# Kernel optimization log

Hardware: AMD Instinct MI355X
Metric: run time of the kernel (lower is better)

The kernel has to match this reference:

```python
import jax, jax.numpy as jnp
import numpy as np

N_NODES = 10000
N_EDGES = 320000
F_IN = 128
HID = 32


def sage_mean(x, src, dst, W_self, W_neigh, b, n_nodes):
    # mean aggregation over in-neighbors (messages flow src -> dst)
    msg = x[src]                                   # [E, F]
    agg = jax.ops.segment_sum(msg, dst, num_segments=n_nodes)   # [N, F]
    deg = jax.ops.segment_sum(jnp.ones((src.shape[0],), x.dtype), dst,
                              num_segments=n_nodes)             # [N]
    h_neigh = agg / jnp.maximum(deg, 1.0)[:, None]
    return x @ W_self + h_neigh @ W_neigh + b


def setup_inputs() -> dict:
    key = jax.random.key(0)
    ks = jax.random.split(key, 12)
    s = 0.05
    return {
        "n_feats": jax.random.normal(ks[0], (N_NODES, F_IN), jnp.float32),
        "src": jax.random.randint(ks[1], (N_EDGES,), 0, N_NODES, jnp.int32),
        "dst": jax.random.randint(ks[2], (N_EDGES,), 0, N_NODES, jnp.int32),
        "eps": jax.random.normal(ks[3], (N_NODES, HID), jnp.float32),
        "W1_self": jax.random.normal(ks[4], (F_IN, HID), jnp.float32) * s,
        "W1_neigh": jax.random.normal(ks[5], (F_IN, HID), jnp.float32) * s,
        "b1": jnp.zeros((HID,), jnp.float32),
        "Wmu_self": jax.random.normal(ks[6], (HID, HID), jnp.float32) * s,
        "Wmu_neigh": jax.random.normal(ks[7], (HID, HID), jnp.float32) * s,
        "bmu": jnp.zeros((HID,), jnp.float32),
        "Wls_self": jax.random.normal(ks[8], (HID, HID), jnp.float32) * s,
        "Wls_neigh": jax.random.normal(ks[9], (HID, HID), jnp.float32) * s,
        "bls": jnp.zeros((HID,), jnp.float32),
    }


def reference(n_feats, src, dst, eps, W1_self, W1_neigh, b1,
              Wmu_self, Wmu_neigh, bmu, Wls_self, Wls_neigh, bls):
    n = n_feats.shape[0]
    h = jax.nn.relu(sage_mean(n_feats, src, dst, W1_self, W1_neigh, b1, n))
    mu = sage_mean(h, src, dst, Wmu_self, Wmu_neigh, bmu, n)
    logstd = sage_mean(h, src, dst, Wls_self, Wls_neigh, bls, n)
    z = mu + eps * jnp.exp(logstd)          # reparameterize
    adj = jax.nn.sigmoid(z @ z.T)           # dot-product decode, [N, N]
    return adj, mu, logstd
```

## Files before the change

kernel.cpp:

```cpp
#include <hip/hip_runtime.h>
#include <hip/hip_bf16.h>


#define N_NODES 10000
#define N_EDGES 320000
#define F_IN 128
#define HID 32

__global__ __launch_bounds__(256) void k_gemm_in(
    const float* __restrict__ x, const float* __restrict__ Ws,
    const float* __restrict__ Wn, const float* __restrict__ b,
    float* __restrict__ outS, float* __restrict__ outN) {
  __shared__ float sWs[F_IN * HID];
  __shared__ float sWn[F_IN * HID];
  __shared__ float sx[8 * F_IN];
  const int t = threadIdx.x;
  for (int i = t * 4; i < F_IN * HID; i += 1024) {
    *(float4*)&sWs[i] = *(const float4*)&Ws[i];
    *(float4*)&sWn[i] = *(const float4*)&Wn[i];
  }
  const int row0 = blockIdx.x * 8;
  {
    const int i = t * 4;
    const int r = i >> 7, k = i & 127;
    const int gr = row0 + r;
    float4 v = make_float4(0.f, 0.f, 0.f, 0.f);
    if (gr < N_NODES) v = *(const float4*)&x[gr * F_IN + k];
    *(float4*)&sx[i] = v;
  }
  __syncthreads();
  const int r = t >> 5, c = t & 31;
  const int grow = row0 + r;
  float accS = 0.f, accN = 0.f;
  #pragma unroll 8
  for (int k = 0; k < F_IN; ++k) {
    const float a = sx[r * F_IN + k];
    accS += a * sWs[k * HID + c];
    accN += a * sWn[k * HID + c];
  }
  if (grow < N_NODES) {
    outS[grow * HID + c] = accS + b[c];
    outN[grow * HID + c] = accN;
  }
}

__global__ __launch_bounds__(256) void k_aggregate(
    const float* __restrict__ feat, const int* __restrict__ src,
    const int* __restrict__ dst, float* __restrict__ agg,
    float* __restrict__ deg) {
  const int tid = blockIdx.x * 256 + threadIdx.x;
  const int e = tid >> 5;
  const int k = tid & 31;
  if (e >= N_EDGES) return;
  const int s = src[e];
  const int d = dst[e];
  atomicAdd(&agg[d * HID + k], feat[s * HID + k]);
  if (deg != nullptr && k == 0) atomicAdd(&deg[d], 1.0f);
}

__global__ __launch_bounds__(256) void k_layer1_finish(
    const float* __restrict__ xws, const float* __restrict__ agg,
    const float* __restrict__ deg, float* __restrict__ h) {
  const int i = blockIdx.x * 256 + threadIdx.x;
  if (i >= N_NODES * HID) return;
  const int node = i >> 5;
  float dv = deg[node];
  dv = dv > 1.f ? dv : 1.f;
  const float v = xws[i] + agg[i] / dv;
  h[i] = v > 0.f ? v : 0.f;
}

__global__ __launch_bounds__(256) void k_layer2(
    const float* __restrict__ h, const float* __restrict__ aggh,
    const float* __restrict__ deg, const float* __restrict__ eps,
    const float* __restrict__ Wms, const float* __restrict__ Wmn,
    const float* __restrict__ bm, const float* __restrict__ Wls,
    const float* __restrict__ Wln, const float* __restrict__ bl,
    float* __restrict__ mu_out, float* __restrict__ ls_out,
    float* __restrict__ z) {
  __shared__ float sMs[HID * HID], sMn[HID * HID];
  __shared__ float sLs[HID * HID], sLn[HID * HID];
  __shared__ float sh[8 * HID], shn[8 * HID];
  const int t = threadIdx.x;
  {
    const int i = t * 4;
    *(float4*)&sMs[i] = *(const float4*)&Wms[i];
    *(float4*)&sMn[i] = *(const float4*)&Wmn[i];
    *(float4*)&sLs[i] = *(const float4*)&Wls[i];
    *(float4*)&sLn[i] = *(const float4*)&Wln[i];
  }
  const int node0 = blockIdx.x * 8;
  const int lr = t >> 5;
  const int gnode_ld = node0 + lr;
  if (gnode_ld < N_NODES) {
    float dv = deg[gnode_ld];
    dv = dv > 1.f ? dv : 1.f;
    sh[t] = h[node0 * HID + t];
    shn[t] = aggh[node0 * HID + t] / dv;
  } else {
    sh[t] = 0.f;
    shn[t] = 0.f;
  }
  __syncthreads();
  const int r = t >> 5, c = t & 31;
  const int node = node0 + r;
  float mu = 0.f, ls = 0.f;
  #pragma unroll 8
  for (int k = 0; k < HID; ++k) {
    const float a = sh[r * HID + k];
    const float an = shn[r * HID + k];
    mu += a * sMs[k * HID + c] + an * sMn[k * HID + c];
    ls += a * sLs[k * HID + c] + an * sLn[k * HID + c];
  }
  if (node < N_NODES) {
    mu += bm[c];
    ls += bl[c];
    const int idx = node * HID + c;
    mu_out[idx] = mu;
    ls_out[idx] = ls;
    z[idx] = mu + eps[idx] * __expf(ls);
  }
}

__global__ __launch_bounds__(256) void k_decode(const float* __restrict__ z,
                                                float* __restrict__ adj) {
  __shared__ float za[128][36];
  __shared__ float zb[128][36];
  const int r0 = blockIdx.y * 128;
  const int c0 = blockIdx.x * 128;
  const int t = threadIdx.x;
  for (int i = t; i < 128 * 8; i += 256) {
    const int row = i >> 3, k0 = (i & 7) << 2;
    const int gr = r0 + row;
    const int gc = c0 + row;
    float4 va = make_float4(0.f, 0.f, 0.f, 0.f);
    float4 vb = make_float4(0.f, 0.f, 0.f, 0.f);
    if (gr < N_NODES) va = *(const float4*)&z[gr * HID + k0];
    if (gc < N_NODES) vb = *(const float4*)&z[gc * HID + k0];
    *(float4*)&za[row][k0] = va;
    *(float4*)&zb[row][k0] = vb;
  }
  __syncthreads();
  const int tx = t & 15, ty = t >> 4;
  float acc[8][8];
  #pragma unroll
  for (int i = 0; i < 8; ++i)
    #pragma unroll
    for (int j = 0; j < 8; ++j) acc[i][j] = 0.f;

  #pragma unroll 4
  for (int k = 0; k < HID; ++k) {
    float a[8], b[8];
    #pragma unroll
    for (int i = 0; i < 8; ++i) a[i] = za[ty + i * 16][k];
    #pragma unroll
    for (int j = 0; j < 8; ++j) b[j] = zb[tx + j * 16][k];
    #pragma unroll
    for (int i = 0; i < 8; ++i)
      #pragma unroll
      for (int j = 0; j < 8; ++j) acc[i][j] += a[i] * b[j];
  }

  #pragma unroll
  for (int i = 0; i < 8; ++i) {
    const int r = r0 + ty + i * 16;
    if (r >= N_NODES) continue;
    float* rowp = adj + (size_t)r * N_NODES;
    #pragma unroll
    for (int j = 0; j < 8; ++j) {
      const int c = c0 + tx + j * 16;
      if (c < N_NODES) {
        const float v = acc[i][j];
        rowp[c] = __builtin_amdgcn_rcpf(1.f + __expf(-v));
      }
    }
  }
}

extern "C" void kernel_launch(void* const* d_in, const int* in_sizes, int n_in,
                              void* d_out, int out_size, void* d_ws,
                              size_t ws_size, hipStream_t stream) {
  const float* x   = (const float*)d_in[0];
  const int* src   = (const int*)d_in[1];
  const int* dst   = (const int*)d_in[2];
  const float* eps = (const float*)d_in[3];
  const float* W1s = (const float*)d_in[4];
  const float* W1n = (const float*)d_in[5];
  const float* b1  = (const float*)d_in[6];
  const float* Wms = (const float*)d_in[7];
  const float* Wmn = (const float*)d_in[8];
  const float* bm  = (const float*)d_in[9];
  const float* Wls = (const float*)d_in[10];
  const float* Wln = (const float*)d_in[11];
  const float* bl  = (const float*)d_in[12];

  float* out = (float*)d_out;
  float* adj = out;
  float* mu_out = out + (size_t)N_NODES * N_NODES;
  float* ls_out = mu_out + (size_t)N_NODES * HID;

  float* ws = (float*)d_ws;
  float* deg  = ws;
  float* agg  = ws + N_NODES;
  float* aggh = agg + N_NODES * HID;
  float* xws  = aggh + N_NODES * HID;
  float* xwn  = xws + N_NODES * HID;
  float* h    = xwn + N_NODES * HID;
  float* z    = h + N_NODES * HID;
  (void)ws_size; (void)in_sizes; (void)n_in; (void)out_size;

  hipMemsetAsync(ws, 0, (size_t)(N_NODES + 2 * N_NODES * HID) * sizeof(float),
                 stream);

  k_gemm_in<<<dim3((N_NODES + 7) / 8), dim3(256), 0, stream>>>(x, W1s, W1n, b1,
                                                               xws, xwn);
  k_aggregate<<<dim3((N_EDGES * HID) / 256), dim3(256), 0, stream>>>(
      xwn, src, dst, agg, deg);
  k_layer1_finish<<<dim3((N_NODES * HID) / 256), dim3(256), 0, stream>>>(
      xws, agg, deg, h);
  k_aggregate<<<dim3((N_EDGES * HID) / 256), dim3(256), 0, stream>>>(
      h, src, dst, aggh, nullptr);
  k_layer2<<<dim3((N_NODES + 7) / 8), dim3(256), 0, stream>>>(
      h, aggh, deg, eps, Wms, Wmn, bm, Wls, Wln, bl, mu_out, ls_out, z);
  dim3 dgrid((N_NODES + 127) / 128, (N_NODES + 127) / 128);
  k_decode<<<dgrid, dim3(256), 0, stream>>>(z, adj);
}
```

Before: 576.3 us.

## Replace atomic edge aggregation with CSR gather and tune GEMM and decode

Builds a CSR by destination (degree count, single-block scan, atomic scatter of sources) and replaces the per-feature float atomicAdd aggregation with per-node gather kernels that fuse mean scaling and, for layer 1, the self term and ReLU. The input GEMM now computes 4 rows per thread, the decode kernel reads its operands from shared memory as float4 and writes adj with nontemporal stores. This removes atomic contention on the feature arrays but adds CSR build kernels, including a serial one-block scan. Neighbour summation order becomes nondeterministic because of the atomic scatter.

```diff
diff --git a/kernel.cpp b/kernel.cpp
--- a/kernel.cpp
+++ b/kernel.cpp
@@ -13,71 +13,135 @@
     float* __restrict__ outS, float* __restrict__ outN) {
   __shared__ float sWs[F_IN * HID];
   __shared__ float sWn[F_IN * HID];
-  __shared__ float sx[8 * F_IN];
-  const int t = threadIdx.x;
+  __shared__ float sx[32 * F_IN];
+  const int t = threadIdx.x;
+  const int node0 = blockIdx.x * 32;
+  #pragma unroll
   for (int i = t * 4; i < F_IN * HID; i += 1024) {
     *(float4*)&sWs[i] = *(const float4*)&Ws[i];
     *(float4*)&sWn[i] = *(const float4*)&Wn[i];
   }
-  const int row0 = blockIdx.x * 8;
-  {
-    const int i = t * 4;
+  #pragma unroll
+  for (int i = t * 4; i < 32 * F_IN; i += 1024) {
     const int r = i >> 7, k = i & 127;
-    const int gr = row0 + r;
+    const int gr = node0 + r;
     float4 v = make_float4(0.f, 0.f, 0.f, 0.f);
     if (gr < N_NODES) v = *(const float4*)&x[gr * F_IN + k];
     *(float4*)&sx[i] = v;
   }
   __syncthreads();
-  const int r = t >> 5, c = t & 31;
-  const int grow = row0 + r;
-  float accS = 0.f, accN = 0.f;
-  #pragma unroll 8
+  const int c = t & 31, g = t >> 5;
+  float accS[4] = {0.f, 0.f, 0.f, 0.f};
+  float accN[4] = {0.f, 0.f, 0.f, 0.f};
+  #pragma unroll 4
   for (int k = 0; k < F_IN; ++k) {
-    const float a = sx[r * F_IN + k];
-    accS += a * sWs[k * HID + c];
-    accN += a * sWn[k * HID + c];
-  }
-  if (grow < N_NODES) {
-    outS[grow * HID + c] = accS + b[c];
-    outN[grow * HID + c] = accN;
-  }
-}
-
-__global__ __launch_bounds__(256) void k_aggregate(
-    const float* __restrict__ feat, const int* __restrict__ src,
-    const int* __restrict__ dst, float* __restrict__ agg,
-    float* __restrict__ deg) {
-  const int tid = blockIdx.x * 256 + threadIdx.x;
-  const int e = tid >> 5;
-  const int k = tid & 31;
+    const float ws = sWs[k * HID + c];
+    const float wn = sWn[k * HID + c];
+    #pragma unroll
+    for (int m = 0; m < 4; ++m) {
+      const float a = sx[(g + 8 * m) * F_IN + k];
+      accS[m] += a * ws;
+      accN[m] += a * wn;
+    }
+  }
+  const float bc = b[c];
+  #pragma unroll
+  for (int m = 0; m < 4; ++m) {
+    const int node = node0 + g + 8 * m;
+    if (node < N_NODES) {
+      outS[node * HID + c] = accS[m] + bc;
+      outN[node * HID + c] = accN[m];
+    }
+  }
+}
+
+__global__ __launch_bounds__(256) void k_degree(const int* __restrict__ dst,
+                                                int* __restrict__ degi) {
+  const int e = blockIdx.x * 256 + threadIdx.x;
+  if (e < N_EDGES) atomicAdd(&degi[dst[e]], 1);
+}
+
+__global__ __launch_bounds__(256) void k_scan(const int* __restrict__ degi,
+                                              int* __restrict__ off,
+                                              int* __restrict__ cursor,
+                                              float* __restrict__ rdeg) {
+  __shared__ int part[256];
+  const int t = threadIdx.x;
+  const int PER = (N_NODES + 255) / 256;
+  const int base = t * PER;
+  int sum = 0;
+  for (int i = 0; i < PER; ++i) {
+    const int idx = base + i;
+    if (idx < N_NODES) sum += degi[idx];
+  }
+  part[t] = sum;
+  __syncthreads();
+  for (int d = 1; d < 256; d <<= 1) {
+    const int v = (t >= d) ? part[t - d] : 0;
+    __syncthreads();
+    part[t] += v;
+    __syncthreads();
+  }
+  int run = (t == 0) ? 0 : part[t - 1];
+  for (int i = 0; i < PER; ++i) {
+    const int idx = base + i;
+    if (idx < N_NODES) {
+      const int d = degi[idx];
+      off[idx] = run;
+      cursor[idx] = run;
+      rdeg[idx] = 1.0f / (float)(d > 1 ? d : 1);
+      run += d;
+    }
+  }
+  if (t == 255) off[N_NODES] = run;
+}
+
+__global__ __launch_bounds__(256) void k_scatter(const int* __restrict__ src,
+                                                 const int* __restrict__ dst,
+                                                 int* __restrict__ cursor,
+                                                 int* __restrict__ esrc) {
+  const int e = blockIdx.x * 256 + threadIdx.x;
   if (e >= N_EDGES) return;
-  const int s = src[e];
-  const int d = dst[e];
-  atomicAdd(&agg[d * HID + k], feat[s * HID + k]);
-  if (deg != nullptr && k == 0) atomicAdd(&deg[d], 1.0f);
-}
-
-__global__ __launch_bounds__(256) void k_layer1_finish(
-    const float* __restrict__ xws, const float* __restrict__ agg,
-    const float* __restrict__ deg, float* __restrict__ h) {
-  const int i = blockIdx.x * 256 + threadIdx.x;
-  if (i >= N_NODES * HID) return;
-  const int node = i >> 5;
-  float dv = deg[node];
-  dv = dv > 1.f ? dv : 1.f;
-  const float v = xws[i] + agg[i] / dv;
-  h[i] = v > 0.f ? v : 0.f;
+  const int pos = atomicAdd(&cursor[dst[e]], 1);
+  esrc[pos] = src[e];
+}
+
+template <bool RELU_ADD>
+__global__ __launch_bounds__(256) void k_gather(
+    const float* __restrict__ feat, const int* __restrict__ off,
+    const int* __restrict__ esrc, const float* __restrict__ rdeg,
+    const float* __restrict__ addend, float* __restrict__ out) {
+  const int t = threadIdx.x;
+  const int node = blockIdx.x * 8 + (t >> 5);
+  const int k = t & 31;
+  if (node >= N_NODES) return;
+  const int j0 = off[node], j1 = off[node + 1];
+  float acc = 0.f;
+  int j = j0;
+  for (; j + 3 < j1; j += 4) {
+    const int s0 = esrc[j], s1 = esrc[j + 1], s2 = esrc[j + 2],
+              s3 = esrc[j + 3];
+    acc += feat[s0 * HID + k];
+    acc += feat[s1 * HID + k];
+    acc += feat[s2 * HID + k];
+    acc += feat[s3 * HID + k];
+  }
+  for (; j < j1; ++j) acc += feat[esrc[j] * HID + k];
+  float v = acc * rdeg[node];
+  if (RELU_ADD) {
+    v += addend[node * HID + k];
+    v = v > 0.f ? v : 0.f;
+  }
+  out[node * HID + k] = v;
 }
 
 __global__ __launch_bounds__(256) void k_layer2(
-    const float* __restrict__ h, const float* __restrict__ aggh,
-    const float* __restrict__ deg, const float* __restrict__ eps,
-    const float* __restrict__ Wms, const float* __restrict__ Wmn,
-    const float* __restrict__ bm, const float* __restrict__ Wls,
-    const float* __restrict__ Wln, const float* __restrict__ bl,
-    float* __restrict__ mu_out, float* __restrict__ ls_out,
-    float* __restrict__ z) {
+    const float* __restrict__ h, const float* __restrict__ hn,
+    const float* __restrict__ eps, const float* __restrict__ Wms,
+    const float* __restrict__ Wmn, const float* __restrict__ bm,
+    const float* __restrict__ Wls, const float* __restrict__ Wln,
+    const float* __restrict__ bl, float* __restrict__ mu_out,
+    float* __restrict__ ls_out, float* __restrict__ z) {
   __shared__ float sMs[HID * HID], sMn[HID * HID];
   __shared__ float sLs[HID * HID], sLn[HID * HID];
   __shared__ float sh[8 * HID], shn[8 * HID];
@@ -90,17 +154,8 @@
     *(float4*)&sLn[i] = *(const float4*)&Wln[i];
   }
   const int node0 = blockIdx.x * 8;
-  const int lr = t >> 5;
-  const int gnode_ld = node0 + lr;
-  if (gnode_ld < N_NODES) {
-    float dv = deg[gnode_ld];
-    dv = dv > 1.f ? dv : 1.f;
-    sh[t] = h[node0 * HID + t];
-    shn[t] = aggh[node0 * HID + t] / dv;
-  } else {
-    sh[t] = 0.f;
-    shn[t] = 0.f;
-  }
+  sh[t] = h[node0 * HID + t];
+  shn[t] = hn[node0 * HID + t];
   __syncthreads();
   const int r = t >> 5, c = t & 31;
   const int node = node0 + r;
@@ -148,17 +203,19 @@
     #pragma unroll
     for (int j = 0; j < 8; ++j) acc[i][j] = 0.f;
 
-  #pragma unroll 4
-  for (int k = 0; k < HID; ++k) {
-    float a[8], b[8];
-    #pragma unroll
-    for (int i = 0; i < 8; ++i) a[i] = za[ty + i * 16][k];
-    #pragma unroll
-    for (int j = 0; j < 8; ++j) b[j] = zb[tx + j * 16][k];
+  #pragma unroll
+  for (int k0 = 0; k0 < HID; k0 += 4) {
+    float4 a4[8], b4[8];
+    #pragma unroll
+    for (int i = 0; i < 8; ++i) a4[i] = *(const float4*)&za[ty + i * 16][k0];
+    #pragma unroll
+    for (int j = 0; j < 8; ++j) b4[j] = *(const float4*)&zb[tx + j * 16][k0];
     #pragma unroll
     for (int i = 0; i < 8; ++i)
       #pragma unroll
-      for (int j = 0; j < 8; ++j) acc[i][j] += a[i] * b[j];
+      for (int j = 0; j < 8; ++j)
+        acc[i][j] += a4[i].x * b4[j].x + a4[i].y * b4[j].y +
+                     a4[i].z * b4[j].z + a4[i].w * b4[j].w;
   }
 
   #pragma unroll
@@ -171,7 +228,8 @@
       const int c = c0 + tx + j * 16;
       if (c < N_NODES) {
         const float v = acc[i][j];
-        rowp[c] = __builtin_amdgcn_rcpf(1.f + __expf(-v));
+        const float s = __builtin_amdgcn_rcpf(1.f + __expf(-v));
+        __builtin_nontemporal_store(s, &rowp[c]);
       }
     }
   }
@@ -199,29 +257,33 @@
   float* mu_out = out + (size_t)N_NODES * N_NODES;
   float* ls_out = mu_out + (size_t)N_NODES * HID;
 
-  float* ws = (float*)d_ws;
-  float* deg  = ws;
-  float* agg  = ws + N_NODES;
-  float* aggh = agg + N_NODES * HID;
-  float* xws  = aggh + N_NODES * HID;
+  char* wsb = (char*)d_ws;
+  int* degi   = (int*)wsb;
+  int* off    = degi + N_NODES;
+  int* cursor = off + N_NODES + 1;
+  int* esrc   = cursor + N_NODES;
+  float* rdeg = (float*)(esrc + N_EDGES);
+  float* xws  = rdeg + N_NODES;
   float* xwn  = xws + N_NODES * HID;
   float* h    = xwn + N_NODES * HID;
-  float* z    = h + N_NODES * HID;
+  float* hn   = h + N_NODES * HID;
+  float* z    = hn + N_NODES * HID;
   (void)ws_size; (void)in_sizes; (void)n_in; (void)out_size;
 
-  hipMemsetAsync(ws, 0, (size_t)(N_NODES + 2 * N_NODES * HID) * sizeof(float),
-                 stream);
-
-  k_gemm_in<<<dim3((N_NODES + 7) / 8), dim3(256), 0, stream>>>(x, W1s, W1n, b1,
-                                                               xws, xwn);
-  k_aggregate<<<dim3((N_EDGES * HID) / 256), dim3(256), 0, stream>>>(
-      xwn, src, dst, agg, deg);
-  k_layer1_finish<<<dim3((N_NODES * HID) / 256), dim3(256), 0, stream>>>(
-      xws, agg, deg, h);
-  k_aggregate<<<dim3((N_EDGES * HID) / 256), dim3(256), 0, stream>>>(
-      h, src, dst, aggh, nullptr);
+  hipMemsetAsync(degi, 0, (size_t)N_NODES * sizeof(int), stream);
+
+  k_gemm_in<<<dim3((N_NODES + 31) / 32), dim3(256), 0, stream>>>(
+      x, W1s, W1n, b1, xws, xwn);
+  k_degree<<<dim3((N_EDGES + 255) / 256), dim3(256), 0, stream>>>(dst, degi);
+  k_scan<<<dim3(1), dim3(256), 0, stream>>>(degi, off, cursor, rdeg);
+  k_scatter<<<dim3((N_EDGES + 255) / 256), dim3(256), 0, stream>>>(
+      src, dst, cursor, esrc);
+  k_gather<true><<<dim3((N_NODES + 7) / 8), dim3(256), 0, stream>>>(
+      xwn, off, esrc, rdeg, xws, h);
+  k_gather<false><<<dim3((N_NODES + 7) / 8), dim3(256), 0, stream>>>(
+      h, off, esrc, rdeg, nullptr, hn);
   k_layer2<<<dim3((N_NODES + 7) / 8), dim3(256), 0, stream>>>(
-      h, aggh, deg, eps, Wms, Wmn, bm, Wls, Wln, bl, mu_out, ls_out, z);
+      h, hn, eps, Wms, Wmn, bm, Wls, Wln, bl, mu_out, ls_out, z);
   dim3 dgrid((N_NODES + 127) / 128, (N_NODES + 127) / 128);
   k_decode<<<dgrid, dim3(256), 0, stream>>>(z, adj);
 }
```

New measurement: 841.7 us. 1.46x slower.
